# Kernel optimization log

Measured on AMD Instinct MI355X. Metric: run time of the kernel, lower is better.

## Reference

```python
import jax, jax.numpy as jnp
import numpy as np

B = 4096          # graphs per batch
SENSORS = 9       # nodes per graph (9*8 = 72 directed edges = 36 pairs x 2)
PAIRS = 36
E_PER_G = 72
HID = 3.0  # unused marker
H = 128
L = 4
EPS = 1e-8


def _build_edge_index():
    # 36 unordered pairs (i<j); per pair emit (i->j) then (j->i) so that
    # reshape(B, 36, 2) groups the two directions of each pair together.
    pairs = [(i, j) for i in range(SENSORS) for j in range(i + 1, SENSORS)]
    rows, cols = [], []
    for i, j in pairs:
        rows += [i, j]
        cols += [j, i]
    rows = np.asarray(rows, np.int32)
    cols = np.asarray(cols, np.int32)
    offs = (np.arange(B, dtype=np.int32) * SENSORS)[:, None]  # [B,1]
    row = (rows[None, :] + offs).reshape(-1)
    col = (cols[None, :] + offs).reshape(-1)
    return jnp.asarray(np.stack([row, col]))  # [2, B*72]


def setup_inputs() -> dict:
    key = jax.random.key(0)
    ks = iter(jax.random.split(key, 32))
    N = B * SENSORS

    def lin(k, fin, fout):
        s = 1.0 / np.sqrt(fin)
        kw, kb = jax.random.split(k)
        return (jax.random.uniform(kw, (fin, fout), jnp.float32, -s, s),
                jax.random.uniform(kb, (fout,), jnp.float32, -s, s))

    x_nodes = jax.random.normal(next(ks), (N, 2), jnp.float32)
    damage_locs = jax.random.normal(next(ks), (B, 2), jnp.float32)
    edge_index = _build_edge_index()
    node_batch = jnp.repeat(jnp.arange(B, dtype=jnp.int32), SENSORS)

    enc_n_w, enc_n_b = lin(next(ks), 2, H)
    enc_e_w1, enc_e_b1 = lin(next(ks), 6, H)
    enc_e_w2, enc_e_b2 = lin(next(ks), H, H)

    ew1, eb1, ew2, eb2, nw1, nb1, nw2, nb2 = [], [], [], [], [], [], [], []
    for _ in range(L):
        w, b = lin(next(ks), 3 * H, H); ew1.append(w); eb1.append(b)
        w, b = lin(next(ks), H, H);     ew2.append(w); eb2.append(b)
        w, b = lin(next(ks), 2 * H, H); nw1.append(w); nb1.append(b)
        w, b = lin(next(ks), H, H);     nw2.append(w); nb2.append(b)
    stk = lambda xs: jnp.stack(xs)

    dec_w1, dec_b1 = lin(next(ks), H, H // 2)
    dec_w2, dec_b2 = lin(next(ks), H // 2, 1)

    return dict(
        x_nodes=x_nodes, damage_locs=damage_locs,
        enc_n_w=enc_n_w, enc_n_b=enc_n_b,
        enc_e_w1=enc_e_w1, enc_e_b1=enc_e_b1, enc_e_w2=enc_e_w2, enc_e_b2=enc_e_b2,
        edge_w1=stk(ew1), edge_b1=stk(eb1), edge_w2=stk(ew2), edge_b2=stk(eb2),
        node_w1=stk(nw1), node_b1=stk(nb1), node_w2=stk(nw2), node_b2=stk(nb2),
        dec_w1=dec_w1, dec_b1=dec_b1, dec_w2=dec_w2, dec_b2=dec_b2,
        edge_index=edge_index, node_batch=node_batch,
    )


def _forward(x_nodes, damage_locs,
             enc_n_w, enc_n_b, enc_e_w1, enc_e_b1, enc_e_w2, enc_e_b2,
             edge_w1, edge_b1, edge_w2, edge_b2,
             node_w1, node_b1, node_w2, node_b2,
             dec_w1, dec_b1, dec_w2, dec_b2,
             edge_index, node_batch):
    N = x_nodes.shape[0]
    row, col = edge_index[0], edge_index[1]
    src = x_nodes[row]                      # [E,2] sender coords (p1)
    dst = x_nodes[col]                      # [E,2] receiver coords (p2)
    dmg = damage_locs[node_batch[row]]      # [E,2] (p3)

    vec = src - dst
    edge_len = jnp.sqrt(jnp.sum(vec * vec, -1, keepdims=True) + EPS)
    d21 = dst - src
    l2 = jnp.clip(jnp.sum(d21 * d21, -1, keepdims=True), EPS, None)
    t = jnp.clip(jnp.sum((dmg - src) * d21, -1, keepdims=True) / l2, 0.0, 1.0)
    proj = src + t * d21
    d_path = jnp.sqrt(jnp.sum((dmg - proj) ** 2, -1, keepdims=True) + EPS)
    d_tx = jnp.sqrt(jnp.sum((src - dmg) ** 2, -1, keepdims=True) + EPS)
    d_rx = jnp.sqrt(jnp.sum((dst - dmg) ** 2, -1, keepdims=True) + EPS)
    phys = jnp.concatenate([vec, edge_len, d_path, d_tx, d_rx], axis=1)  # [E,6]

    h_n = x_nodes @ enc_n_w + enc_n_b
    h_e = jax.nn.relu(phys @ enc_e_w1 + enc_e_b1) @ enc_e_w2 + enc_e_b2

    ones = jnp.ones((row.shape[0],), h_n.dtype)
    deg = jnp.clip(jax.ops.segment_sum(ones, col, num_segments=N), 1.0, None)[:, None]

    for l in range(L):
        ein = jnp.concatenate([h_n[row], h_n[col], h_e], axis=1)  # [E,3H]
        h_e = h_e + jax.nn.relu(ein @ edge_w1[l] + edge_b1[l]) @ edge_w2[l] + edge_b2[l]
        # PyG default message(x_j): mean of sender node features at receiver
        agg = jax.ops.segment_sum(h_n[row], col, num_segments=N) / deg
        nin = jnp.concatenate([h_n, agg], axis=1)                 # [N,2H]
        h_n = h_n + jax.nn.relu(nin @ node_w1[l] + node_b1[l]) @ node_w2[l] + node_b2[l]

    dec = jax.nn.sigmoid(jax.nn.relu(h_e @ dec_w1 + dec_b1) @ dec_w2 + dec_b2)  # [E,1]
    return dec.reshape(B, PAIRS, 2).mean(axis=2)  # [B,36]


def reference(x_nodes, damage_locs,
              enc_n_w, enc_n_b, enc_e_w1, enc_e_b1, enc_e_w2, enc_e_b2,
              edge_w1, edge_b1, edge_w2, edge_b2,
              node_w1, node_b1, node_w2, node_b2,
              dec_w1, dec_b1, dec_w2, dec_b2,
              edge_index, node_batch):
    return _forward(x_nodes, damage_locs,
                    enc_n_w, enc_n_b, enc_e_w1, enc_e_b1, enc_e_w2, enc_e_b2,
                    edge_w1, edge_b1, edge_w2, edge_b2,
                    node_w1, node_b1, node_w2, node_b2,
                    dec_w1, dec_b1, dec_w2, dec_b2,
                    edge_index, node_batch)
```

## Files before the change

### kernel.cpp

```cpp
#include <hip/hip_runtime.h>
#include <math.h>

typedef unsigned short u16;
typedef __attribute__((ext_vector_type(8))) short bf16x8;
typedef __attribute__((ext_vector_type(4))) float f32x4;

#define NSENS 9
#define NEDGE 72
#define NPAIR 36
#define HDIM 128
#define NLAYER 4
#define FEPS 1e-8f

#define ST    136
#define STNIN 264
#define STPH  40

__device__ __forceinline__ u16 f2bf(float f) {
    unsigned u = __float_as_uint(f);
    return (u16)((u + 0x7FFFu + ((u >> 16) & 1u)) >> 16);
}
__device__ __forceinline__ float bf2f(u16 h) { return __uint_as_float(((unsigned)h) << 16); }
__device__ __forceinline__ unsigned pkbf(float lo, float hi) {
    return ((unsigned)f2bf(hi) << 16) | (unsigned)f2bf(lo);
}

#define SZ_EE1 (1*8*512)
#define SZ_EE2 (4*8*512)
#define SZ_EW1 (12*8*512)
#define SZ_EW2 (4*8*512)
#define SZ_NW1 (8*8*512)
#define SZ_NW2 (4*8*512)
#define SZ_DW1 (4*4*512)
#define OFF_EE1 0
#define OFF_EE2 (OFF_EE1 + SZ_EE1)
#define OFF_EW1 (OFF_EE2 + SZ_EE2)
#define OFF_EW2 (OFF_EW1 + 4*SZ_EW1)
#define OFF_NW1 (OFF_EW2 + 4*SZ_EW2)
#define OFF_NW2 (OFF_NW1 + 4*SZ_NW1)
#define OFF_DW1 (OFF_NW2 + 4*SZ_NW2)

__device__ __forceinline__ void pack_one(const float* __restrict__ s, u16* __restrict__ d,
                                         int Ksrc, int N, int NT, int kbnt) {
    const int kb = kbnt / NT, nt = kbnt % NT;
    const int ln = threadIdx.x, q = ln >> 4, c = ln & 15;
    const int n  = nt * 16 + c;
    u16* dp = d + ((kb * NT + nt) * 64 + ln) * 8;
#pragma unroll
    for (int j = 0; j < 8; ++j) {
        int k = kb * 32 + q * 8 + j;
        dp[j] = f2bf((k < Ksrc) ? s[k * N + n] : 0.f);
    }
}

__global__ void pack_all(const float* __restrict__ ee1, const float* __restrict__ ee2,
                         const float* __restrict__ ew1, const float* __restrict__ ew2,
                         const float* __restrict__ nw1, const float* __restrict__ nw2,
                         const float* __restrict__ dw1, u16* __restrict__ ws) {
    int b = blockIdx.x;
    if (b < 8)        { pack_one(ee1, ws + OFF_EE1, 6, 128, 8, b); return; }
    b -= 8;
    if (b < 32)       { pack_one(ee2, ws + OFF_EE2, 128, 128, 8, b); return; }
    b -= 32;
    if (b < 384)      { int l = b / 96;
                        pack_one(ew1 + l*384*128, ws + OFF_EW1 + l*SZ_EW1, 384, 128, 8, b % 96); return; }
    b -= 384;
    if (b < 128)      { int l = b / 32;
                        pack_one(ew2 + l*128*128, ws + OFF_EW2 + l*SZ_EW2, 128, 128, 8, b % 32); return; }
    b -= 128;
    if (b < 256)      { int l = b / 64;
                        pack_one(nw1 + l*256*128, ws + OFF_NW1 + l*SZ_NW1, 256, 128, 8, b % 64); return; }
    b -= 256;
    if (b < 128)      { int l = b / 32;
                        pack_one(nw2 + l*128*128, ws + OFF_NW2 + l*SZ_NW2, 128, 128, 8, b % 32); return; }
    b -= 128;
    pack_one(dw1, ws + OFF_DW1, 128, 64, 4, b);
}

template<int NMT, int NKB, int NT, typename FA>
__device__ __forceinline__ void wave_gemm(const u16* __restrict__ Wp, int nt, int ln,
                                          FA fa, f32x4* acc) {
    const u16* wp = Wp + (nt * 64 + ln) * 8;
#pragma unroll
    for (int kb = 0; kb < NKB; ++kb) {
        bf16x8 b = *(const bf16x8*)(wp + kb * NT * 512);
#pragma unroll
        for (int mt = 0; mt < NMT; ++mt) {
            bf16x8 a = fa(mt, kb);
            acc[mt] = __builtin_amdgcn_mfma_f32_16x16x32_bf16(a, b, acc[mt], 0, 0, 0);
        }
    }
}

#define ZACC(A, N) do { _Pragma("unroll") for (int _i = 0; _i < (N); ++_i) \
                        (A)[_i] = (f32x4){0.f, 0.f, 0.f, 0.f}; } while (0)

extern "C" __global__ void __launch_bounds__(512, 2)
gnn_mfma(const float* __restrict__ x_nodes, const float* __restrict__ damage_locs,
         const float* __restrict__ enc_n_w, const float* __restrict__ enc_n_b,
         const float* __restrict__ enc_e_b1, const float* __restrict__ enc_e_b2,
         const float* __restrict__ edge_b1, const float* __restrict__ edge_b2,
         const float* __restrict__ node_b1, const float* __restrict__ node_b2,
         const float* __restrict__ dec_b1, const float* __restrict__ dec_w2,
         const float* __restrict__ dec_b2,
         const u16* __restrict__ wpack, float* __restrict__ out)
{
    __shared__ __align__(16) u16 smem[192 * ST];
    __shared__ float s_x[NSENS * 2];
    __shared__ float s_dmg[2];
    __shared__ float s_val[NEDGE];
    __shared__ int s_src[NEDGE], s_dst[NEDGE];

    u16* b_he  = smem;
    u16* b_t   = smem + 80 * ST;
    u16* b_hn  = smem + 160 * ST;
    u16* b_nt  = smem + 176 * ST;
    u16* b_ph  = b_he;
    u16* b_nin = b_t;

    const int g   = blockIdx.x;
    const int tid = threadIdx.x;
    const int wv  = tid >> 6, ln = tid & 63;
    const int q   = ln >> 4,  cl = ln & 15;
    const int col = wv * 16 + cl;

    auto stp = [&](u16* buf, int stride, int c, int Rb, int Rlim,
                   float v0, float v1, float v2, float v3) {
        const bool od = cl & 1;
        float x = od ? v0 : v2, y = od ? v1 : v3;
        float px = __shfl_xor(x, 1), py = __shfl_xor(y, 1);
        float lo0 = od ? px : v0, hi0 = od ? v2 : px;
        float lo1 = od ? py : v1, hi1 = od ? v3 : py;
        const int r0 = Rb + (od ? 2 : 0);
        const int cc = c & ~1;
        if (r0 < Rlim)     *(unsigned*)(buf + r0 * stride + cc)       = pkbf(lo0, hi0);
        if (r0 + 1 < Rlim) *(unsigned*)(buf + (r0 + 1) * stride + cc) = pkbf(lo1, hi1);
    };

    {
        uint4 z = {0, 0, 0, 0};
        uint4* zp = (uint4*)smem;
        for (int i = tid; i < (192 * ST * 2) / 16; i += 512) zp[i] = z;
    }
    if (tid < NSENS * 2) s_x[tid] = x_nodes[g * NSENS * 2 + tid];
    if (tid < 2)         s_dmg[tid] = damage_locs[g * 2 + tid];
    if (tid < NEDGE) {
        int p = tid >> 1;
        int i = 0, rem = p, cnt = 8;
        while (rem >= cnt) { rem -= cnt; --cnt; ++i; }
        int j = i + 1 + rem;
        s_src[tid] = (tid & 1) ? j : i;
        s_dst[tid] = (tid & 1) ? i : j;
    }
    __syncthreads();

    if (tid < NEDGE) {
        const int si = s_src[tid], di = s_dst[tid];
        const float sx = s_x[2*si], sy = s_x[2*si+1];
        const float dx = s_x[2*di], dy = s_x[2*di+1];
        const float gx = s_dmg[0],  gy = s_dmg[1];
        const float vx = sx - dx, vy = sy - dy;
        const float vv = vx*vx + vy*vy;
        const float elen = sqrtf(vv + FEPS);
        const float l2 = fmaxf(vv, FEPS);
        float t = ((gx - sx) * (dx - sx) + (gy - sy) * (dy - sy)) / l2;
        t = fminf(fmaxf(t, 0.f), 1.f);
        const float px = sx + t * (dx - sx), py = sy + t * (dy - sy);
        u16* ph = b_ph + tid * STPH;
        ph[0] = f2bf(vx); ph[1] = f2bf(vy); ph[2] = f2bf(elen);
        ph[3] = f2bf(sqrtf((gx-px)*(gx-px) + (gy-py)*(gy-py) + FEPS));
        ph[4] = f2bf(sqrtf((sx-gx)*(sx-gx) + (sy-gy)*(sy-gy) + FEPS));
        ph[5] = f2bf(sqrtf((dx-gx)*(dx-gx) + (dy-gy)*(dy-gy) + FEPS));
    }

    f32x4 m_hn;
    {
        const float w0 = enc_n_w[col], w1 = enc_n_w[HDIM + col], bb = enc_n_b[col];
#pragma unroll
        for (int r = 0; r < 4; ++r) {
            const int R = q * 4 + r;
            m_hn[r] = (R < NSENS) ? fmaf(s_x[2*R], w0, fmaf(s_x[2*R+1], w1, bb)) : 0.f;
        }
        stp(b_hn, ST, col, q * 4, NSENS, m_hn[0], m_hn[1], m_hn[2], m_hn[3]);
    }

    int rowS[5], rowD[5], rowE[5];
#pragma unroll
    for (int mt = 0; mt < 5; ++mt) {
        int e = mt * 16 + cl; if (e >= NEDGE) e = NEDGE - 1;
        rowS[mt] = s_src[e] * ST; rowD[mt] = s_dst[e] * ST; rowE[mt] = e * ST;
    }
    __syncthreads();

    auto fa_t   = [&](int mt, int kb) -> bf16x8 {
        return *(const bf16x8*)(b_t + (mt * 16 + cl) * ST + kb * 32 + q * 8); };
    auto fa_ph  = [&](int mt, int kb) -> bf16x8 {
        return *(const bf16x8*)(b_ph + (mt * 16 + cl) * STPH + q * 8); };
    auto fa_nin = [&](int mt, int kb) -> bf16x8 {
        return *(const bf16x8*)(b_nin + cl * STNIN + kb * 32 + q * 8); };
    auto fa_nt  = [&](int mt, int kb) -> bf16x8 {
        return *(const bf16x8*)(b_nt + cl * ST + kb * 32 + q * 8); };
    auto fa_ein = [&](int mt, int kb) -> bf16x8 {
        const u16* p;
        if (kb < 4)      p = b_hn + rowS[mt] + kb * 32;
        else if (kb < 8) p = b_hn + rowD[mt] + (kb - 4) * 32;
        else             p = b_he + rowE[mt] + (kb - 8) * 32;
        return *(const bf16x8*)(p + q * 8); };

    f32x4 m_he[5];

    {
        f32x4 acc[5]; ZACC(acc, 5);
        wave_gemm<5, 1, 8>(wpack + OFF_EE1, wv, ln, fa_ph, acc);
        const float bb = enc_e_b1[col];
#pragma unroll
        for (int mt = 0; mt < 5; ++mt)
            stp(b_t, ST, col, mt * 16 + q * 4, NEDGE,
                fmaxf(acc[mt][0] + bb, 0.f), fmaxf(acc[mt][1] + bb, 0.f),
                fmaxf(acc[mt][2] + bb, 0.f), fmaxf(acc[mt][3] + bb, 0.f));
    }
    __syncthreads();
    {
        f32x4 acc[5]; ZACC(acc, 5);
        wave_gemm<5, 4, 8>(wpack + OFF_EE2, wv, ln, fa_t, acc);
        const float bb = enc_e_b2[col];
#pragma unroll
        for (int mt = 0; mt < 5; ++mt) {
#pragma unroll
            for (int r = 0; r < 4; ++r) m_he[mt][r] = acc[mt][r] + bb;
            stp(b_he, ST, col, mt * 16 + q * 4, NEDGE,
                m_he[mt][0], m_he[mt][1], m_he[mt][2], m_he[mt][3]);
        }
    }
    __syncthreads();

    for (int l = 0; l < NLAYER; ++l) {
        {
            f32x4 acc[5]; ZACC(acc, 5);
            wave_gemm<5, 12, 8>(wpack + OFF_EW1 + l * SZ_EW1, wv, ln, fa_ein, acc);
            const float bb = edge_b1[l * HDIM + col];
#pragma unroll
            for (int mt = 0; mt < 5; ++mt)
                stp(b_t, ST, col, mt * 16 + q * 4, NEDGE,
                    fmaxf(acc[mt][0] + bb, 0.f), fmaxf(acc[mt][1] + bb, 0.f),
                    fmaxf(acc[mt][2] + bb, 0.f), fmaxf(acc[mt][3] + bb, 0.f));
        }
        __syncthreads();
        {
            f32x4 acc[5]; ZACC(acc, 5);
            wave_gemm<5, 4, 8>(wpack + OFF_EW2 + l * SZ_EW2, wv, ln, fa_t, acc);
            const float bb = edge_b2[l * HDIM + col];
#pragma unroll
            for (int mt = 0; mt < 5; ++mt) {
#pragma unroll
                for (int r = 0; r < 4; ++r) m_he[mt][r] += acc[mt][r] + bb;
                stp(b_he, ST, col, mt * 16 + q * 4, NEDGE,
                    m_he[mt][0], m_he[mt][1], m_he[mt][2], m_he[mt][3]);
            }
        }
        __syncthreads();
        {
            float p4 = m_hn[0] + m_hn[1] + m_hn[2] + m_hn[3];
            p4 += __shfl_xor(p4, 16);
            p4 += __shfl_xor(p4, 32);
            stp(b_nin, STNIN, col, q * 4, NSENS, m_hn[0], m_hn[1], m_hn[2], m_hn[3]);
            stp(b_nin, STNIN, HDIM + col, q * 4, NSENS,
                (p4 - m_hn[0]) * 0.125f, (p4 - m_hn[1]) * 0.125f,
                (p4 - m_hn[2]) * 0.125f, (p4 - m_hn[3]) * 0.125f);
        }
        __syncthreads();
        {
            f32x4 acc[1]; ZACC(acc, 1);
            wave_gemm<1, 8, 8>(wpack + OFF_NW1 + l * SZ_NW1, wv, ln, fa_nin, acc);
            const float bb = node_b1[l * HDIM + col];
            stp(b_nt, ST, col, q * 4, 16,
                fmaxf(acc[0][0] + bb, 0.f), fmaxf(acc[0][1] + bb, 0.f),
                fmaxf(acc[0][2] + bb, 0.f), fmaxf(acc[0][3] + bb, 0.f));
        }
        __syncthreads();
        {
            f32x4 acc[1]; ZACC(acc, 1);
            wave_gemm<1, 4, 8>(wpack + OFF_NW2 + l * SZ_NW2, wv, ln, fa_nt, acc);
            const float bb = node_b2[l * HDIM + col];
#pragma unroll
            for (int r = 0; r < 4; ++r)
                if (q * 4 + r < NSENS) m_hn[r] += acc[0][r] + bb;
            stp(b_hn, ST, col, q * 4, NSENS, m_hn[0], m_hn[1], m_hn[2], m_hn[3]);
        }
        __syncthreads();
    }

    {
        const int ntd = wv & 3;
        const int mt0 = (wv < 4) ? 0 : 2;
        f32x4 acc[3]; ZACC(acc, 3);
        auto fa_d = [&](int mt, int kb) -> bf16x8 {
            return *(const bf16x8*)(b_he + ((mt0 + mt) * 16 + cl) * ST + kb * 32 + q * 8); };
        wave_gemm<3, 4, 4>(wpack + OFF_DW1, ntd, ln, fa_d, acc);
        const int c64 = ntd * 16 + cl;
        const float bb = dec_b1[c64];
#pragma unroll
        for (int mt = 0; mt < 3; ++mt)
            stp(b_t, ST, c64, (mt0 + mt) * 16 + q * 4, NEDGE,
                fmaxf(acc[mt][0] + bb, 0.f), fmaxf(acc[mt][1] + bb, 0.f),
                fmaxf(acc[mt][2] + bb, 0.f), fmaxf(acc[mt][3] + bb, 0.f));
    }
    __syncthreads();
    if (tid < NEDGE) {
        float a = dec_b2[0];
        const u16* tt = b_t + tid * ST;
#pragma unroll
        for (int k = 0; k < 64; ++k) a = fmaf(bf2f(tt[k]), dec_w2[k], a);
        s_val[tid] = 1.f / (1.f + expf(-a));
    }
    __syncthreads();
    if (tid < NPAIR)
        out[g * NPAIR + tid] = 0.5f * (s_val[2 * tid] + s_val[2 * tid + 1]);
}

extern "C" void kernel_launch(void* const* d_in, const int* in_sizes, int n_in,
                              void* d_out, int out_size, void* d_ws, size_t ws_size,
                              hipStream_t stream) {
    const float* x_nodes     = (const float*)d_in[0];
    const float* damage_locs = (const float*)d_in[1];
    const float* enc_n_w  = (const float*)d_in[2];
    const float* enc_n_b  = (const float*)d_in[3];
    const float* enc_e_w1 = (const float*)d_in[4];
    const float* enc_e_b1 = (const float*)d_in[5];
    const float* enc_e_w2 = (const float*)d_in[6];
    const float* enc_e_b2 = (const float*)d_in[7];
    const float* edge_w1  = (const float*)d_in[8];
    const float* edge_b1  = (const float*)d_in[9];
    const float* edge_w2  = (const float*)d_in[10];
    const float* edge_b2  = (const float*)d_in[11];
    const float* node_w1  = (const float*)d_in[12];
    const float* node_b1  = (const float*)d_in[13];
    const float* node_w2  = (const float*)d_in[14];
    const float* node_b2  = (const float*)d_in[15];
    const float* dec_w1   = (const float*)d_in[16];
    const float* dec_b1   = (const float*)d_in[17];
    const float* dec_w2   = (const float*)d_in[18];
    const float* dec_b2   = (const float*)d_in[19];
    float* out = (float*)d_out;
    u16* ws = (u16*)d_ws;

    hipLaunchKernelGGL(pack_all, dim3(952), dim3(64), 0, stream,
                       enc_e_w1, enc_e_w2, edge_w1, edge_w2, node_w1, node_w2, dec_w1, ws);

    const int ngraph = in_sizes[1] / 2;
    hipLaunchKernelGGL(gnn_mfma, dim3(ngraph), dim3(512), 0, stream,
                       x_nodes, damage_locs, enc_n_w, enc_n_b,
                       enc_e_b1, enc_e_b2, edge_b1, edge_b2,
                       node_b1, node_b2, dec_b1, dec_w2, dec_b2,
                       ws, out);
}
```

Before: 402.2 us.

## Seed accumulators with bias, prefetch weights, shrink LDS, simplify bf16 stores

Accumulators are initialized with the bias so the epilogue add disappears. The B-operand weight load is software-prefetched one k-block ahead. The node-temp buffer is moved inside the b_t region so shared memory shrinks, and only the phase buffer is zeroed at startup. The shuffle-based packed bf16 store is replaced by a hardware packed convert plus four 16-bit scalar stores. Trade-offs: more, narrower LDS writes, and possible subtle differences in rounding and padding behavior.

```diff
diff --git a/kernel.cpp b/kernel.cpp
--- a/kernel.cpp
+++ b/kernel.cpp
@@ -21,8 +21,19 @@
     return (u16)((u + 0x7FFFu + ((u >> 16) & 1u)) >> 16);
 }
 __device__ __forceinline__ float bf2f(u16 h) { return __uint_as_float(((unsigned)h) << 16); }
-__device__ __forceinline__ unsigned pkbf(float lo, float hi) {
+
+__device__ __forceinline__ unsigned cvt2(float lo, float hi) {
+#if defined(__has_builtin)
+#if __has_builtin(__builtin_amdgcn_cvt_pk_bf16_f32)
+    typedef __attribute__((ext_vector_type(2))) __bf16 bf16x2_t;
+    bf16x2_t t = __builtin_amdgcn_cvt_pk_bf16_f32(lo, hi);
+    unsigned u; __builtin_memcpy(&u, &t, 4); return u;
+#else
     return ((unsigned)f2bf(hi) << 16) | (unsigned)f2bf(lo);
+#endif
+#else
+    return ((unsigned)f2bf(hi) << 16) | (unsigned)f2bf(lo);
+#endif
 }
 
 #define SZ_EE1 (1*8*512)
@@ -81,19 +92,22 @@
 __device__ __forceinline__ void wave_gemm(const u16* __restrict__ Wp, int nt, int ln,
                                           FA fa, f32x4* acc) {
     const u16* wp = Wp + (nt * 64 + ln) * 8;
+    bf16x8 bc = *(const bf16x8*)(wp);
 #pragma unroll
     for (int kb = 0; kb < NKB; ++kb) {
-        bf16x8 b = *(const bf16x8*)(wp + kb * NT * 512);
+        bf16x8 bn;
+        if (kb + 1 < NKB) bn = *(const bf16x8*)(wp + (kb + 1) * NT * 512);
 #pragma unroll
         for (int mt = 0; mt < NMT; ++mt) {
             bf16x8 a = fa(mt, kb);
-            acc[mt] = __builtin_amdgcn_mfma_f32_16x16x32_bf16(a, b, acc[mt], 0, 0, 0);
-        }
-    }
-}
-
-#define ZACC(A, N) do { _Pragma("unroll") for (int _i = 0; _i < (N); ++_i) \
-                        (A)[_i] = (f32x4){0.f, 0.f, 0.f, 0.f}; } while (0)
+            acc[mt] = __builtin_amdgcn_mfma_f32_16x16x32_bf16(a, bc, acc[mt], 0, 0, 0);
+        }
+        if (kb + 1 < NKB) bc = bn;
+    }
+}
+
+#define BACC(A, N, b) do { _Pragma("unroll") for (int _i = 0; _i < (N); ++_i) \
+                           (A)[_i] = (f32x4){(b), (b), (b), (b)}; } while (0)
 
 extern "C" __global__ void __launch_bounds__(512, 2)
 gnn_mfma(const float* __restrict__ x_nodes, const float* __restrict__ damage_locs,
@@ -105,7 +119,7 @@
          const float* __restrict__ dec_b2,
          const u16* __restrict__ wpack, float* __restrict__ out)
 {
-    __shared__ __align__(16) u16 smem[192 * ST];
+    __shared__ __align__(16) u16 smem[176 * ST];
     __shared__ float s_x[NSENS * 2];
     __shared__ float s_dmg[2];
     __shared__ float s_val[NEDGE];
@@ -114,9 +128,9 @@
     u16* b_he  = smem;
     u16* b_t   = smem + 80 * ST;
     u16* b_hn  = smem + 160 * ST;
-    u16* b_nt  = smem + 176 * ST;
     u16* b_ph  = b_he;
     u16* b_nin = b_t;
+    u16* b_nt  = b_t + 48 * ST;
 
     const int g   = blockIdx.x;
     const int tid = threadIdx.x;
@@ -124,23 +138,19 @@
     const int q   = ln >> 4,  cl = ln & 15;
     const int col = wv * 16 + cl;
 
-    auto stp = [&](u16* buf, int stride, int c, int Rb, int Rlim,
+    auto st4 = [&](u16* buf, int stride, int c, int Rb, int Rlim,
                    float v0, float v1, float v2, float v3) {
-        const bool od = cl & 1;
-        float x = od ? v0 : v2, y = od ? v1 : v3;
-        float px = __shfl_xor(x, 1), py = __shfl_xor(y, 1);
-        float lo0 = od ? px : v0, hi0 = od ? v2 : px;
-        float lo1 = od ? py : v1, hi1 = od ? v3 : py;
-        const int r0 = Rb + (od ? 2 : 0);
-        const int cc = c & ~1;
-        if (r0 < Rlim)     *(unsigned*)(buf + r0 * stride + cc)       = pkbf(lo0, hi0);
-        if (r0 + 1 < Rlim) *(unsigned*)(buf + (r0 + 1) * stride + cc) = pkbf(lo1, hi1);
+        unsigned d01 = cvt2(v0, v1), d23 = cvt2(v2, v3);
+        if (Rb + 0 < Rlim) buf[(Rb + 0) * stride + c] = (u16)d01;
+        if (Rb + 1 < Rlim) buf[(Rb + 1) * stride + c] = (u16)(d01 >> 16);
+        if (Rb + 2 < Rlim) buf[(Rb + 2) * stride + c] = (u16)d23;
+        if (Rb + 3 < Rlim) buf[(Rb + 3) * stride + c] = (u16)(d23 >> 16);
     };
 
     {
         uint4 z = {0, 0, 0, 0};
-        uint4* zp = (uint4*)smem;
-        for (int i = tid; i < (192 * ST * 2) / 16; i += 512) zp[i] = z;
+        uint4* zp = (uint4*)b_ph;
+        for (int i = tid; i < (80 * STPH * 2) / 16; i += 512) zp[i] = z;
     }
     if (tid < NSENS * 2) s_x[tid] = x_nodes[g * NSENS * 2 + tid];
     if (tid < 2)         s_dmg[tid] = damage_locs[g * 2 + tid];
@@ -181,7 +191,7 @@
             const int R = q * 4 + r;
             m_hn[r] = (R < NSENS) ? fmaf(s_x[2*R], w0, fmaf(s_x[2*R+1], w1, bb)) : 0.f;
         }
-        stp(b_hn, ST, col, q * 4, NSENS, m_hn[0], m_hn[1], m_hn[2], m_hn[3]);
+        st4(b_hn, ST, col, q * 4, NSENS, m_hn[0], m_hn[1], m_hn[2], m_hn[3]);
     }
 
     int rowS[5], rowD[5], rowE[5];
@@ -210,25 +220,22 @@
     f32x4 m_he[5];
 
     {
-        f32x4 acc[5]; ZACC(acc, 5);
+        f32x4 acc[5]; BACC(acc, 5, enc_e_b1[col]);
         wave_gemm<5, 1, 8>(wpack + OFF_EE1, wv, ln, fa_ph, acc);
-        const float bb = enc_e_b1[col];
 #pragma unroll
         for (int mt = 0; mt < 5; ++mt)
-            stp(b_t, ST, col, mt * 16 + q * 4, NEDGE,
-                fmaxf(acc[mt][0] + bb, 0.f), fmaxf(acc[mt][1] + bb, 0.f),
-                fmaxf(acc[mt][2] + bb, 0.f), fmaxf(acc[mt][3] + bb, 0.f));
-    }
-    __syncthreads();
-    {
-        f32x4 acc[5]; ZACC(acc, 5);
+            st4(b_t, ST, col, mt * 16 + q * 4, NEDGE,
+                fmaxf(acc[mt][0], 0.f), fmaxf(acc[mt][1], 0.f),
+                fmaxf(acc[mt][2], 0.f), fmaxf(acc[mt][3], 0.f));
+    }
+    __syncthreads();
+    {
+        f32x4 acc[5]; BACC(acc, 5, enc_e_b2[col]);
         wave_gemm<5, 4, 8>(wpack + OFF_EE2, wv, ln, fa_t, acc);
-        const float bb = enc_e_b2[col];
 #pragma unroll
         for (int mt = 0; mt < 5; ++mt) {
-#pragma unroll
-            for (int r = 0; r < 4; ++r) m_he[mt][r] = acc[mt][r] + bb;
-            stp(b_he, ST, col, mt * 16 + q * 4, NEDGE,
+            m_he[mt] = acc[mt];
+            st4(b_he, ST, col, mt * 16 + q * 4, NEDGE,
                 m_he[mt][0], m_he[mt][1], m_he[mt][2], m_he[mt][3]);
         }
     }
@@ -236,25 +243,23 @@
 
     for (int l = 0; l < NLAYER; ++l) {
         {
-            f32x4 acc[5]; ZACC(acc, 5);
+            f32x4 acc[5]; BACC(acc, 5, edge_b1[l * HDIM + col]);
             wave_gemm<5, 12, 8>(wpack + OFF_EW1 + l * SZ_EW1, wv, ln, fa_ein, acc);
-            const float bb = edge_b1[l * HDIM + col];
 #pragma unroll
             for (int mt = 0; mt < 5; ++mt)
-                stp(b_t, ST, col, mt * 16 + q * 4, NEDGE,
-                    fmaxf(acc[mt][0] + bb, 0.f), fmaxf(acc[mt][1] + bb, 0.f),
-                    fmaxf(acc[mt][2] + bb, 0.f), fmaxf(acc[mt][3] + bb, 0.f));
-        }
-        __syncthreads();
-        {
-            f32x4 acc[5]; ZACC(acc, 5);
+                st4(b_t, ST, col, mt * 16 + q * 4, NEDGE,
+                    fmaxf(acc[mt][0], 0.f), fmaxf(acc[mt][1], 0.f),
+                    fmaxf(acc[mt][2], 0.f), fmaxf(acc[mt][3], 0.f));
+        }
+        __syncthreads();
+        {
+            f32x4 acc[5]; BACC(acc, 5, edge_b2[l * HDIM + col]);
             wave_gemm<5, 4, 8>(wpack + OFF_EW2 + l * SZ_EW2, wv, ln, fa_t, acc);
-            const float bb = edge_b2[l * HDIM + col];
 #pragma unroll
             for (int mt = 0; mt < 5; ++mt) {
 #pragma unroll
-                for (int r = 0; r < 4; ++r) m_he[mt][r] += acc[mt][r] + bb;
-                stp(b_he, ST, col, mt * 16 + q * 4, NEDGE,
+                for (int r = 0; r < 4; ++r) m_he[mt][r] += acc[mt][r];
+                st4(b_he, ST, col, mt * 16 + q * 4, NEDGE,
                     m_he[mt][0], m_he[mt][1], m_he[mt][2], m_he[mt][3]);
             }
         }
@@ -263,29 +268,27 @@
             float p4 = m_hn[0] + m_hn[1] + m_hn[2] + m_hn[3];
             p4 += __shfl_xor(p4, 16);
             p4 += __shfl_xor(p4, 32);
-            stp(b_nin, STNIN, col, q * 4, NSENS, m_hn[0], m_hn[1], m_hn[2], m_hn[3]);
-            stp(b_nin, STNIN, HDIM + col, q * 4, NSENS,
+            st4(b_nin, STNIN, col, q * 4, NSENS, m_hn[0], m_hn[1], m_hn[2], m_hn[3]);
+            st4(b_nin, STNIN, HDIM + col, q * 4, NSENS,
                 (p4 - m_hn[0]) * 0.125f, (p4 - m_hn[1]) * 0.125f,
                 (p4 - m_hn[2]) * 0.125f, (p4 - m_hn[3]) * 0.125f);
         }
         __syncthreads();
         {
-            f32x4 acc[1]; ZACC(acc, 1);
+            f32x4 acc[1]; BACC(acc, 1, node_b1[l * HDIM + col]);
             wave_gemm<1, 8, 8>(wpack + OFF_NW1 + l * SZ_NW1, wv, ln, fa_nin, acc);
-            const float bb = node_b1[l * HDIM + col];
-            stp(b_nt, ST, col, q * 4, 16,
-                fmaxf(acc[0][0] + bb, 0.f), fmaxf(acc[0][1] + bb, 0.f),
-                fmaxf(acc[0][2] + bb, 0.f), fmaxf(acc[0][3] + bb, 0.f));
-        }
-        __syncthreads();
-        {
-            f32x4 acc[1]; ZACC(acc, 1);
+            st4(b_nt, ST, col, q * 4, 16,
+                fmaxf(acc[0][0], 0.f), fmaxf(acc[0][1], 0.f),
+                fmaxf(acc[0][2], 0.f), fmaxf(acc[0][3], 0.f));
+        }
+        __syncthreads();
+        {
+            f32x4 acc[1]; BACC(acc, 1, node_b2[l * HDIM + col]);
             wave_gemm<1, 4, 8>(wpack + OFF_NW2 + l * SZ_NW2, wv, ln, fa_nt, acc);
-            const float bb = node_b2[l * HDIM + col];
 #pragma unroll
             for (int r = 0; r < 4; ++r)
-                if (q * 4 + r < NSENS) m_hn[r] += acc[0][r] + bb;
-            stp(b_hn, ST, col, q * 4, NSENS, m_hn[0], m_hn[1], m_hn[2], m_hn[3]);
+                if (q * 4 + r < NSENS) m_hn[r] += acc[0][r];
+            st4(b_hn, ST, col, q * 4, NSENS, m_hn[0], m_hn[1], m_hn[2], m_hn[3]);
         }
         __syncthreads();
     }
@@ -293,17 +296,16 @@
     {
         const int ntd = wv & 3;
         const int mt0 = (wv < 4) ? 0 : 2;
-        f32x4 acc[3]; ZACC(acc, 3);
         auto fa_d = [&](int mt, int kb) -> bf16x8 {
             return *(const bf16x8*)(b_he + ((mt0 + mt) * 16 + cl) * ST + kb * 32 + q * 8); };
+        const int c64 = ntd * 16 + cl;
+        f32x4 acc[3]; BACC(acc, 3, dec_b1[c64]);
         wave_gemm<3, 4, 4>(wpack + OFF_DW1, ntd, ln, fa_d, acc);
-        const int c64 = ntd * 16 + cl;
-        const float bb = dec_b1[c64];
 #pragma unroll
         for (int mt = 0; mt < 3; ++mt)
-            stp(b_t, ST, c64, (mt0 + mt) * 16 + q * 4, NEDGE,
-                fmaxf(acc[mt][0] + bb, 0.f), fmaxf(acc[mt][1] + bb, 0.f),
-                fmaxf(acc[mt][2] + bb, 0.f), fmaxf(acc[mt][3] + bb, 0.f));
+            st4(b_t, ST, c64, (mt0 + mt) * 16 + q * 4, NEDGE,
+                fmaxf(acc[mt][0], 0.f), fmaxf(acc[mt][1], 0.f),
+                fmaxf(acc[mt][2], 0.f), fmaxf(acc[mt][3], 0.f));
     }
     __syncthreads();
     if (tid < NEDGE) {
```

Result: faster. 373.6 us (-7.1%).
